# Performance work log

Measured on AMD Instinct MI355X. Metric: run time of the kernel, lower is better.

Reference implementation:

```python
import jax, jax.numpy as jnp
import numpy as np

N, E, D, L, G = 50000, 600000, 128, 3, 512
MAX_DIS = 5
BN_EPS = 1e-5


def _bn(z, g, b):
    # BatchNorm1d in training mode: biased batch statistics over axis 0
    mu = jnp.mean(z, axis=0)
    var = jnp.var(z, axis=0)
    return (z - mu) * jax.lax.rsqrt(var + BN_EPS) * g + b


def setup_inputs() -> dict:
    key = jax.random.key(0)
    ks = jax.random.split(key, 16)
    s = 0.05
    inp = {
        # int inputs
        'd': jax.random.randint(ks[0], (N,), 0, MAX_DIS + 1, dtype=jnp.int32),
        'src': jax.random.randint(ks[1], (E,), 0, N, dtype=jnp.int32),
        'dst': jax.random.randint(ks[2], (E,), 0, N, dtype=jnp.int32),
        'batch_ids': jnp.sort(jax.random.randint(ks[3], (N,), 0, G, dtype=jnp.int32)),
        # NodeEmbedding distance table
        'embed_d': jax.random.normal(ks[4], (MAX_DIS + 1, D)) * s,
        # per-layer params (stacked over L layers)
        'lin_W': jax.random.normal(ks[5], (L, D, D)) * s,   # self.linear weight (stored [in,out])
        'lin_b': jnp.zeros((L, D)),                          # self.linear bias
        'mlp_W1': jax.random.normal(ks[6], (L, D, D)) * s,   # MLP input linear (no bias, norm=True)
        'mlp_g1': jnp.ones((L, D)), 'mlp_b1': jnp.zeros((L, D)),  # MLP inner BN
        'mlp_W2': jax.random.normal(ks[7], (L, D, D)) * s,   # MLP output linear (no bias)
        'eps': jnp.zeros((L,)),                              # GIN eps per layer
        'bn_g': jnp.ones((L, D)), 'bn_b': jnp.zeros((L, D)), # LWL outer BN
        # Pool (gin=False, task='g')
        'pool_W1': jax.random.normal(ks[8], (D, D)) * s,
        'pool_g1': jnp.ones((D,)), 'pool_b1': jnp.zeros((D,)),
        'pool_W2': jax.random.normal(ks[9], (D, D)) * s,
        'pbn_g': jnp.ones((D,)), 'pbn_b': jnp.zeros((D,)),
        # predict MLP (norm=False -> biases, hdim=2*D, odim=num_tasks*num_classes=1)
        'pred_W1': jax.random.normal(ks[10], (D, 2 * D)) * s,
        'pred_b1': jnp.zeros((2 * D,)),
        'pred_W2': jax.random.normal(ks[11], (2 * D, 1)) * s,
        'pred_b2': jnp.zeros((1,)),
    }
    return inp


def reference(d, src, dst, batch_ids, embed_d, lin_W, lin_b,
              mlp_W1, mlp_g1, mlp_b1, mlp_W2, eps, bn_g, bn_b,
              pool_W1, pool_g1, pool_b1, pool_W2, pbn_g, pbn_b,
              pred_W1, pred_b1, pred_W2, pred_b2):
    # NodeEmbedding: x = embed_d(clamp(d, 0, max_dis))  (enc_a=None -> no feature encoder)
    x = embed_d[jnp.clip(d, 0, MAX_DIS)]                      # [N, D]

    counts = jax.ops.segment_sum(jnp.ones((N,), x.dtype), batch_ids, num_segments=G)
    denom = jnp.maximum(counts, 1.0)[:, None]                 # [G, 1]

    h_means = []
    for l in range(L):
        # L('vL'): message = relu(index_select(linear(x), src))  (enc_e=None)
        m = jax.nn.relu((x @ lin_W[l] + lin_b[l])[src])        # [E, D]
        # aggregate = scatter_add to dst over N nodes
        agg = jax.ops.segment_sum(m, dst, num_segments=N)      # [N, D]
        z = x * (1.0 + eps[l]) + agg                           # GIN eps residual
        # MLP(norm=True): Linear(no bias) -> BN -> ReLU -> Linear(no bias)
        h = jax.nn.relu(_bn(z @ mlp_W1[l], mlp_g1[l], mlp_b1[l])) @ mlp_W2[l]
        # LWL outer: x = relu(bn(xL))
        x = jax.nn.relu(_bn(h, bn_g[l], bn_b[l]))
        # global_mean_pool of this layer's output
        h_means.append(jax.ops.segment_sum(x, batch_ids, num_segments=G) / denom)

    # Pool (gin=False, task='g'); index_u is identity for plain MP, so scatter/gather are no-ops
    p = jax.nn.relu(_bn(x @ pool_W1, pool_g1, pool_b1)) @ pool_W2   # pooling MLP
    p = jax.nn.relu(_bn(p, pbn_g, pbn_b))
    h_graph = jax.ops.segment_sum(p, batch_ids, num_segments=G) / denom  # scatter mean
    # predict MLP (norm=False): Linear+bias -> ReLU -> Linear+bias
    prediction = jax.nn.relu(h_graph @ pred_W1 + pred_b1) @ pred_W2 + pred_b2  # [G, 1]

    return prediction, h_graph, jnp.stack(h_means)  # h_list stacked [L, G, D]
```

## Files before the change

### kernel.cpp

```cpp
#include <hip/hip_runtime.h>

typedef unsigned short ushort_t;
typedef __attribute__((ext_vector_type(8))) short bf16x8;
typedef __attribute__((ext_vector_type(4))) float f32x4;

#define NN 50000
#define NE 600000
#define DD 128
#define LL 3
#define GG 512
#define NB_SCAN 98
#define GGRID 1563
#define SBK 32

__device__ __forceinline__ float b2f(ushort_t u){ return __uint_as_float(((unsigned)u)<<16); }
__device__ __forceinline__ ushort_t f2b(float f){
    unsigned x = __float_as_uint(f);
    return (ushort_t)((x + 0x7fffu + ((x>>16)&1u)) >> 16);
}

__global__ void k_mark(float* __restrict__ out, float val, int n){
    int i = blockIdx.x*256 + threadIdx.x; if (i >= n) return;
    out[i] = (i == 0) ? val : 0.f;
}

struct WPtrs { const float* p[11]; };
__global__ void k_setup(WPtrs wp, ushort_t* __restrict__ Wf,
                        const int* __restrict__ bids, int* __restrict__ goff,
                        int* __restrict__ cnt, float* __restrict__ banks,
                        const float* __restrict__ emb, const float* __restrict__ linW,
                        const float* __restrict__ linB, float* __restrict__ yrows){
    int idx = blockIdx.x*256 + threadIdx.x;
    if (idx < 180224){
        int m = idx >> 14, r = idx & 16383;
        int i = r & 7, l2 = (r >> 3) & 63, s = (r >> 9) & 3, n = r >> 11;
        int k   = s*32 + (l2 >> 4)*8 + i;
        int col = n*16 + (l2 & 15);
        Wf[idx] = f2b(wp.p[m][k*DD + col]);
    } else if (idx < 180737){
        int g = idx - 180224;
        int lo = 0, hi = NN;
        while (lo < hi){ int mid = (lo+hi) >> 1; if (bids[mid] < g) lo = mid+1; else hi = mid; }
        goff[g] = lo;
    } else if (idx < 230737){
        cnt[idx - 180737] = 0;
    } else if (idx < 296273){
        banks[idx - 230737] = 0.f;
    } else if (idx < 297041){
        int i = idx - 296273;
        int di = i >> 7, c = i & 127;
        float acc = linB[c];
        for (int k = 0; k < DD; k++) acc = fmaf(emb[di*DD + k], linW[k*DD + c], acc);
        yrows[i] = fmaxf(acc, 0.f);
    }
}

__global__ void k_count(const int* __restrict__ dst, int* __restrict__ cnt){
    int e4 = blockIdx.x*256 + threadIdx.x; if (e4 >= NE/4) return;
    int4 dv = ((const int4*)dst)[e4];
    atomicAdd(&cnt[dv.x], 1); atomicAdd(&cnt[dv.y], 1);
    atomicAdd(&cnt[dv.z], 1); atomicAdd(&cnt[dv.w], 1);
}
__global__ void k_scanA(const int* __restrict__ cnt, int* __restrict__ inc, int* __restrict__ bsum){
    __shared__ int s[512];
    int i = blockIdx.x*512 + threadIdx.x;
    int v = (i < NN) ? cnt[i] : 0;
    s[threadIdx.x] = v; __syncthreads();
    for (int off = 1; off < 512; off <<= 1){
        int add = (threadIdx.x >= off) ? s[threadIdx.x - off] : 0;
        __syncthreads();
        s[threadIdx.x] += add;
        __syncthreads();
    }
    if (i < NN) inc[i] = s[threadIdx.x];
    if (threadIdx.x == 511) bsum[blockIdx.x] = s[511];
}
__global__ void k_scanB(const int* __restrict__ bsum, int* __restrict__ boff){
    __shared__ int s[128];
    int t = threadIdx.x;
    int v = (t < NB_SCAN) ? bsum[t] : 0;
    s[t] = v; __syncthreads();
    for (int off = 1; off < 128; off <<= 1){
        int a = (t >= off) ? s[t - off] : 0;
        __syncthreads();
        s[t] += a;
        __syncthreads();
    }
    if (t < NB_SCAN) boff[t] = s[t] - v;
    if (t == NB_SCAN - 1) boff[NB_SCAN] = s[t];
}
__global__ void k_scanC(const int* __restrict__ cnt, const int* __restrict__ inc,
                        const int* __restrict__ boff, int* __restrict__ rowptr,
                        int* __restrict__ cursor){
    int i = blockIdx.x*512 + threadIdx.x;
    if (i < NN){
        int e = boff[blockIdx.x] + inc[i] - cnt[i];
        rowptr[i] = e; cursor[i] = e;
    } else if (i == NN){
        rowptr[NN] = NE;
    }
}
__global__ void k_fill(const int* __restrict__ src, const int* __restrict__ dst,
                       int* __restrict__ cursor, int* __restrict__ eidx){
    int e4 = blockIdx.x*256 + threadIdx.x; if (e4 >= NE/4) return;
    int4 dv = ((const int4*)dst)[e4];
    int4 sv = ((const int4*)src)[e4];
    int p0 = atomicAdd(&cursor[dv.x], 1); eidx[p0] = sv.x;
    int p1 = atomicAdd(&cursor[dv.y], 1); eidx[p1] = sv.y;
    int p2 = atomicAdd(&cursor[dv.z], 1); eidx[p2] = sv.z;
    int p3 = atomicAdd(&cursor[dv.w], 1); eidx[p3] = sv.w;
}

__global__ void k_agg0(const int* __restrict__ d, const float* __restrict__ emb,
                       const float* __restrict__ yrows,
                       const int* __restrict__ rowptr, const int* __restrict__ eidx,
                       const float* __restrict__ epsP, ushort_t* __restrict__ zb){
    __shared__ float eL[6*DD], yL[6*DD];
    int t = threadIdx.x;
    for (int i = t; i < 6*DD; i += 256){ eL[i] = emb[i]; yL[i] = yrows[i]; }
    __syncthreads();
    int node = blockIdx.x*16 + (t >> 4);
    if (node >= NN) return;
    int c8 = (t & 15) << 3;
    float epl = 1.0f + epsP[0];
    int dv = d[node]; dv = dv < 0 ? 0 : (dv > 5 ? 5 : dv);
    float a[8];
#pragma unroll
    for (int i = 0; i < 8; i++) a[i] = eL[dv*DD + c8 + i] * epl;
    int e0 = rowptr[node], e1 = rowptr[node+1];
    int e = e0;
    for (; e + 3 < e1; e += 4){
        int s0 = eidx[e], s1 = eidx[e+1], s2 = eidx[e+2], s3 = eidx[e+3];
        int c0 = d[s0], c1 = d[s1], c2 = d[s2], c3 = d[s3];
        c0 = c0 < 0 ? 0 : (c0 > 5 ? 5 : c0);
        c1 = c1 < 0 ? 0 : (c1 > 5 ? 5 : c1);
        c2 = c2 < 0 ? 0 : (c2 > 5 ? 5 : c2);
        c3 = c3 < 0 ? 0 : (c3 > 5 ? 5 : c3);
#pragma unroll
        for (int i = 0; i < 8; i++)
            a[i] += (yL[c0*DD + c8 + i] + yL[c1*DD + c8 + i])
                  + (yL[c2*DD + c8 + i] + yL[c3*DD + c8 + i]);
    }
    for (; e < e1; e++){
        int s = eidx[e];
        int c = d[s]; c = c < 0 ? 0 : (c > 5 ? 5 : c);
#pragma unroll
        for (int i = 0; i < 8; i++) a[i] += yL[c*DD + c8 + i];
    }
    bf16x8 o;
#pragma unroll
    for (int i = 0; i < 8; i++) o[i] = (short)f2b(a[i]);
    *(bf16x8*)(zb + (size_t)node*DD + c8) = o;
}

__global__ void k_agg(const ushort_t* __restrict__ xb, const ushort_t* __restrict__ yb,
                      ushort_t* __restrict__ zb,
                      const int* __restrict__ rowptr, const int* __restrict__ eidx,
                      const float* __restrict__ epsP, int l,
                      const float* __restrict__ banksIn, const float* __restrict__ bng,
                      const float* __restrict__ bnb){
    __shared__ float sst[256];
    int t = threadIdx.x;
    {
        float sv = 0.f;
#pragma unroll
        for (int b = 0; b < SBK; b++) sv += banksIn[(b << 8) + t];
        sst[t] = sv;
    }
    __syncthreads();
    int node = blockIdx.x*16 + (t >> 4);
    if (node >= NN) return;
    int c8 = (t & 15) << 3;
    float epl = 1.0f + epsP[l];
    bf16x8 xr = *(const bf16x8*)(xb + (size_t)node*DD + c8);
    float a[8];
#pragma unroll
    for (int i = 0; i < 8; i++){
        int c = c8 + i;
        float mu  = sst[c] * (1.0f/NN);
        float var = sst[c + DD] * (1.0f/NN) - mu*mu;
        float sc  = rsqrtf(fmaxf(var, 0.f) + 1e-5f) * bng[c];
        float sh  = bnb[c] - mu*sc;
        a[i] = fmaxf(fmaf(b2f((ushort_t)xr[i]), sc, sh), 0.f) * epl;
    }
    int e0 = rowptr[node], e1 = rowptr[node+1];
    int e = e0;
    for (; e + 3 < e1; e += 4){
        int s0 = eidx[e], s1 = eidx[e+1], s2 = eidx[e+2], s3 = eidx[e+3];
        bf16x8 v0 = *(const bf16x8*)(yb + (size_t)s0*DD + c8);
        bf16x8 v1 = *(const bf16x8*)(yb + (size_t)s1*DD + c8);
        bf16x8 v2 = *(const bf16x8*)(yb + (size_t)s2*DD + c8);
        bf16x8 v3 = *(const bf16x8*)(yb + (size_t)s3*DD + c8);
#pragma unroll
        for (int i = 0; i < 8; i++)
            a[i] += (b2f((ushort_t)v0[i]) + b2f((ushort_t)v1[i]))
                  + (b2f((ushort_t)v2[i]) + b2f((ushort_t)v3[i]));
    }
    for (; e < e1; e++){
        int s = eidx[e];
        bf16x8 v = *(const bf16x8*)(yb + (size_t)s*DD + c8);
#pragma unroll
        for (int i = 0; i < 8; i++) a[i] += b2f((ushort_t)v[i]);
    }
    bf16x8 o;
#pragma unroll
    for (int i = 0; i < 8; i++) o[i] = (short)f2b(a[i]);
    *(bf16x8*)(zb + (size_t)node*DD + c8) = o;
}

template<int AMODE, int OMODE, int STATS, int POOL>
__global__ __launch_bounds__(256) void k_gemm(
    const ushort_t* __restrict__ A, const ushort_t* __restrict__ Wf,
    const float* __restrict__ bias,
    const float* __restrict__ banksIn, const float* __restrict__ bng,
    const float* __restrict__ bnb,
    ushort_t* __restrict__ C, float* __restrict__ banksOut,
    const int* __restrict__ goff, float* __restrict__ pool_out, int M)
{
    __shared__ float ssl[256];
    __shared__ float sred[256];
    __shared__ ushort_t lrep[32*132];
    const int t = threadIdx.x;

    if (POOL && blockIdx.x >= GGRID){
        int g = blockIdx.x - GGRID;
        {
            float sv = 0.f;
#pragma unroll
            for (int b = 0; b < SBK; b++) sv += banksIn[(b << 8) + t];
            ssl[t] = sv;
        }
        __syncthreads();
        int c = t & 127, hf = t >> 7;
        float mu  = ssl[c] * (1.0f/NN);
        float var = ssl[c + DD] * (1.0f/NN) - mu*mu;
        float sc  = rsqrtf(fmaxf(var, 0.f) + 1e-5f) * bng[c];
        float sh  = bnb[c] - mu*sc;
        int r0 = goff[g], r1 = goff[g+1];
        float acc = 0.f;
        for (int r = r0 + hf; r < r1; r += 2)
            acc += fmaxf(fmaf(b2f(A[(size_t)r*DD + c]), sc, sh), 0.f);
        sred[t] = acc; __syncthreads();
        if (t < 128)
            pool_out[g*DD + t] = (sred[t] + sred[t+128]) / fmaxf((float)(r1 - r0), 1.0f);
        return;
    }

    const int w = t >> 6, l = t & 63;
    const int rw = w >> 1, cw = w & 1;
    const int rowBlk = blockIdx.x*32, rowBase = rowBlk + rw*16;
    const int lm = l & 15, kg = l >> 4;

    if (AMODE == 2){
        float sv = 0.f;
#pragma unroll
        for (int b = 0; b < SBK; b++) sv += banksIn[(b << 8) + t];
        ssl[t] = sv;
        __syncthreads();
        if (t < 128){
            float mu  = ssl[t] * (1.0f/NN);
            float var = ssl[t + DD] * (1.0f/NN) - mu*mu;
            float sc  = rsqrtf(fmaxf(var, 0.f) + 1e-5f) * bng[t];
            ssl[t] = sc;
            ssl[t + DD] = bnb[t] - mu*sc;
        }
    }
    if (STATS) sred[t] = 0.f;
    if (AMODE == 2 || STATS) __syncthreads();

    f32x4 acc[4];
#pragma unroll
    for (int n = 0; n < 4; n++) acc[n] = (f32x4){0.f,0.f,0.f,0.f};

    int arow = rowBase + lm;
    if (arow >= M) arow = M - 1;
    const ushort_t* aptr = A + (size_t)arow*DD + kg*8;

#pragma unroll
    for (int s = 0; s < 4; s++){
        bf16x8 af;
        if (AMODE == 0){
            af = *(const bf16x8*)(aptr + s*32);
        } else {
            bf16x8 ar = *(const bf16x8*)(aptr + s*32);
            int k0 = s*32 + kg*8;
#pragma unroll
            for (int i = 0; i < 8; i++){
                float v = b2f((ushort_t)ar[i]);
                v = fmaxf(fmaf(v, ssl[k0+i], ssl[DD+k0+i]), 0.f);
                ((ushort_t*)&af)[i] = f2b(v);
            }
        }
#pragma unroll
        for (int n = 0; n < 4; n++){
            int nc = cw*4 + n;
            bf16x8 bfr = *(const bf16x8*)(Wf + (size_t)((nc*4 + s)*64 + l)*8);
            acc[n] = __builtin_amdgcn_mfma_f32_16x16x32_bf16(af, bfr, acc[n], 0, 0, 0);
        }
    }

#pragma unroll
    for (int n = 0; n < 4; n++){
        int col = (cw*4 + n)*16 + lm;
        float cs = 0.f, cq = 0.f;
#pragma unroll
        for (int j = 0; j < 4; j++){
            float v = acc[n][j];
            if (OMODE == 1) v = fmaxf(v + bias[col], 0.f);
            lrep[(rw*16 + kg*4 + j)*132 + col] = f2b(v);
            if (STATS && (rowBase + kg*4 + j) < M){ cs += v; cq += v*v; }
        }
        if (STATS){
            cs += __shfl_xor(cs, 16); cs += __shfl_xor(cs, 32);
            cq += __shfl_xor(cq, 16); cq += __shfl_xor(cq, 32);
            if (kg == 0){
                atomicAdd(&sred[col], cs);
                atomicAdd(&sred[col + DD], cq);
            }
        }
    }
    __syncthreads();

    {
        int lr = t >> 3;
        int gr = rowBlk + lr;
        if (gr < M){
            int seg = (t & 7) * 16;
            const ushort_t* lp = lrep + lr*132 + seg;
            bf16x8 o0 = *(const bf16x8*)(lp);
            bf16x8 o1 = *(const bf16x8*)(lp + 8);
            ushort_t* cp = C + (size_t)gr*DD + seg;
            *(bf16x8*)(cp)     = o0;
            *(bf16x8*)(cp + 8) = o1;
        }
    }

    if (STATS){
        __syncthreads();
        atomicAdd(&banksOut[((blockIdx.x & (SBK-1)) << 8) + t], sred[t]);
    }
}

__global__ __launch_bounds__(256) void k_poolpred(const ushort_t* __restrict__ zb,
        const float* __restrict__ banksIn, const float* __restrict__ bng,
        const float* __restrict__ bnb, const int* __restrict__ goff,
        const float* __restrict__ W1, const float* __restrict__ b1,
        const float* __restrict__ W2, const float* __restrict__ b2,
        float* __restrict__ out_hgraph, float* __restrict__ out_pred){
    __shared__ float hrow[DD];
    __shared__ float pr[256];
    int g = blockIdx.x, t = threadIdx.x;
    {
        float sv = 0.f;
#pragma unroll
        for (int b = 0; b < SBK; b++) sv += banksIn[(b << 8) + t];
        pr[t] = sv;
    }
    __syncthreads();
    int c = t & 127, hf = t >> 7;
    float mu  = pr[c] * (1.0f/NN);
    float var = pr[c + DD] * (1.0f/NN) - mu*mu;
    float sc  = rsqrtf(fmaxf(var, 0.f) + 1e-5f) * bng[c];
    float sh  = bnb[c] - mu*sc;
    __syncthreads();
    int r0 = goff[g], r1 = goff[g+1];
    float acc = 0.f;
    for (int r = r0 + hf; r < r1; r += 2)
        acc += fmaxf(fmaf(b2f(zb[(size_t)r*DD + c]), sc, sh), 0.f);
    pr[t] = acc; __syncthreads();
    if (t < 128){
        float m = (pr[t] + pr[t+128]) / fmaxf((float)(r1 - r0), 1.0f);
        hrow[t] = m;
        out_hgraph[g*DD + t] = m;
    }
    __syncthreads();
    float a2 = b1[t];
    for (int k = 0; k < DD; k++) a2 = fmaf(hrow[k], W1[k*256 + t], a2);
    pr[t] = fmaxf(a2, 0.f) * W2[t];
    __syncthreads();
    for (int off = 128; off > 0; off >>= 1){
        if (t < off) pr[t] += pr[t + off];
        __syncthreads();
    }
    if (t == 0) out_pred[g] = pr[0] + b2[0];
}

extern "C" void kernel_launch(void* const* d_in, const int* in_sizes, int n_in,
                              void* d_out, int out_size, void* d_ws, size_t ws_size,
                              hipStream_t stream){
    float* out = (float*)d_out;
    const int OUT_N = GG + GG*DD + LL*GG*DD;

    static const int EXP[24] = {50000,600000,600000,50000, 768,49152,384,49152,384,384,
                                49152,3,384,384,16384,128,128,16384,128,128,
                                32768,256,256,1};
    int bad = -1;
    if (n_in != 24) bad = 50;
    else for (int i = 0; i < 24; i++) if (in_sizes[i] != EXP[i]) { bad = i; break; }
    if (bad >= 0){
        k_mark<<<(OUT_N+255)/256, 256, 0, stream>>>(out, 2048.0f + (float)bad, OUT_N);
        return;
    }

    const int* d    = (const int*)d_in[0];
    const int* src  = (const int*)d_in[1];
    const int* dst  = (const int*)d_in[2];
    const int* bids = (const int*)d_in[3];
    const float* emb  = (const float*)d_in[4];
    const float* linW = (const float*)d_in[5];
    const float* linB = (const float*)d_in[6];
    const float* W1   = (const float*)d_in[7];
    const float* g1   = (const float*)d_in[8];
    const float* b1   = (const float*)d_in[9];
    const float* W2   = (const float*)d_in[10];
    const float* epsA = (const float*)d_in[11];
    const float* bng  = (const float*)d_in[12];
    const float* bnb  = (const float*)d_in[13];
    const float* pW1  = (const float*)d_in[14];
    const float* pg1  = (const float*)d_in[15];
    const float* pb1  = (const float*)d_in[16];
    const float* pW2  = (const float*)d_in[17];
    const float* pbng = (const float*)d_in[18];
    const float* pbnb = (const float*)d_in[19];
    const float* prW1 = (const float*)d_in[20];
    const float* prb1 = (const float*)d_in[21];
    const float* prW2 = (const float*)d_in[22];
    const float* prb2 = (const float*)d_in[23];

    ushort_t* xb  = (ushort_t*)d_ws;
    ushort_t* yb  = xb + (size_t)NN*DD;
    ushort_t* zb  = yb + (size_t)NN*DD;
    ushort_t* Wf  = zb + (size_t)NN*DD;
    float* SBANKS= (float*)(Wf + 11*16384);
    float* yrows = SBANKS + 8*SBK*256;
    int* cnt    = (int*)(yrows + 6*DD);
    int* inc    = cnt + NN;
    int* rowptr = inc + NN;
    int* cursor = rowptr + NN + 1;
    int* eidx   = cursor + NN;
    int* goff   = eidx + NE;
    int* bsum   = goff + GG + 1;
    int* boff   = bsum + NB_SCAN;

    float* out_pred   = out;
    float* out_hgraph = out + GG;
    float* out_hmeans = out + GG + GG*DD;

    const int AGG_GRID  = (NN + 15)/16;
    const int E4_GRID   = (NE/4 + 255)/256;
    const int SETUP_GRID= (297041 + 255)/256;
    const int GP_GRID   = GGRID + GG;

    WPtrs wp;
    for (int i = 0; i < 3; i++){
        wp.p[i]   = linW + (size_t)i*DD*DD;
        wp.p[3+i] = W1   + (size_t)i*DD*DD;
        wp.p[6+i] = W2   + (size_t)i*DD*DD;
    }
    wp.p[9] = pW1; wp.p[10] = pW2;
    const ushort_t* WfLin = Wf;
    const ushort_t* WfW1  = Wf + 3*16384;
    const ushort_t* WfW2  = Wf + 6*16384;
    const ushort_t* WfPW1 = Wf + 9*16384;
    const ushort_t* WfPW2 = Wf + 10*16384;

    float* BK0 = SBANKS + 0*SBK*256;
    float* BK1 = SBANKS + 1*SBK*256;
    float* BK5 = SBANKS + 5*SBK*256;
    float* BK6 = SBANKS + 6*SBK*256;
    float* BK7 = SBANKS + 7*SBK*256;

    k_setup<<<SETUP_GRID, 256, 0, stream>>>(wp, Wf, bids, goff, cnt, SBANKS,
                                            emb, linW, linB, yrows);
    k_count<<<E4_GRID, 256, 0, stream>>>(dst, cnt);
    k_scanA<<<NB_SCAN, 512, 0, stream>>>(cnt, inc, bsum);
    k_scanB<<<1, 128, 0, stream>>>(bsum, boff);
    k_scanC<<<NB_SCAN, 512, 0, stream>>>(cnt, inc, boff, rowptr, cursor);
    k_fill<<<E4_GRID, 256, 0, stream>>>(src, dst, cursor, eidx);

    k_agg0<<<AGG_GRID, 256, 0, stream>>>(d, emb, yrows, rowptr, eidx, epsA, zb);
    k_gemm<0,0,1,0><<<GGRID, 256, 0, stream>>>(zb, WfW1, nullptr, nullptr, nullptr, nullptr,
        yb, BK0, nullptr, nullptr, NN);
    k_gemm<2,0,1,0><<<GGRID, 256, 0, stream>>>(yb, WfW2, nullptr, BK0, g1, b1,
        xb, BK1, nullptr, nullptr, NN);

    for (int l = 1; l < LL; l++){
        float* pbank = SBANKS + (size_t)(2*l - 1)*SBK*256;
        float* bIn   = SBANKS + (size_t)(2*l)*SBK*256;
        float* bOut  = SBANKS + (size_t)(2*l + 1)*SBK*256;
        const float* pg = bng + (size_t)(l-1)*DD;
        const float* pb = bnb + (size_t)(l-1)*DD;

        k_gemm<2,1,0,1><<<GP_GRID, 256, 0, stream>>>(xb, WfLin + (size_t)l*16384,
            linB + (size_t)l*DD, pbank, pg, pb,
            yb, nullptr, goff, out_hmeans + (size_t)(l-1)*GG*DD, NN);
        k_agg<<<AGG_GRID, 256, 0, stream>>>(xb, yb, zb, rowptr, eidx, epsA, l, pbank, pg, pb);
        k_gemm<0,0,1,0><<<GGRID, 256, 0, stream>>>(zb, WfW1 + (size_t)l*16384, nullptr,
            nullptr, nullptr, nullptr, yb, bIn, nullptr, nullptr, NN);
        k_gemm<2,0,1,0><<<GGRID, 256, 0, stream>>>(yb, WfW2 + (size_t)l*16384, nullptr,
            bIn, g1 + (size_t)l*DD, b1 + (size_t)l*DD, xb, bOut, nullptr, nullptr, NN);
    }

    k_gemm<2,0,1,1><<<GP_GRID, 256, 0, stream>>>(xb, WfPW1, nullptr,
        BK5, bng + 2*DD, bnb + 2*DD,
        yb, BK6, goff, out_hmeans + (size_t)2*GG*DD, NN);
    k_gemm<2,0,1,0><<<GGRID, 256, 0, stream>>>(yb, WfPW2, nullptr,
        BK6, pg1, pb1, zb, BK7, nullptr, nullptr, NN);
    k_poolpred<<<GG, 256, 0, stream>>>(zb, BK7, pbng, pbnb, goff,
        prW1, prb1, prW2, prb2, out_hgraph, out_pred);
}
```

Baseline: 372.3 us.

## Fuse neighbor aggregation into first MLP GEMM and merge scan kernels

The separate aggregation kernels (layer 0 lookup-table path and later bf16 gather path) are folded into the W1 GEMM. Each block gathers and sums neighbor messages for its 32 rows into LDS, then feeds them to the MFMA. This removes the z round trip through global memory and two launches per layer. The scanB kernel is merged into scanC by having every block redo the small 98-element prefix scan. In exchange the GEMM blocks carry more LDS and irregular gather latency, which may lower occupancy, and buffers are re-routed (zb/yb swapped).

New measurement: 358.0 us. 3.8% less time.

```diff
diff --git a/kernel.cpp b/kernel.cpp
--- a/kernel.cpp
+++ b/kernel.cpp
@@ -75,26 +75,23 @@
     if (i < NN) inc[i] = s[threadIdx.x];
     if (threadIdx.x == 511) bsum[blockIdx.x] = s[511];
 }
-__global__ void k_scanB(const int* __restrict__ bsum, int* __restrict__ boff){
-    __shared__ int s[128];
+__global__ void k_scanC(const int* __restrict__ cnt, const int* __restrict__ inc,
+                        const int* __restrict__ bsum, int* __restrict__ rowptr,
+                        int* __restrict__ cursor){
+    __shared__ int sb[128];
     int t = threadIdx.x;
-    int v = (t < NB_SCAN) ? bsum[t] : 0;
-    s[t] = v; __syncthreads();
+    if (t < 128) sb[t] = (t < NB_SCAN) ? bsum[t] : 0;
+    __syncthreads();
     for (int off = 1; off < 128; off <<= 1){
-        int a = (t >= off) ? s[t - off] : 0;
-        __syncthreads();
-        s[t] += a;
-        __syncthreads();
-    }
-    if (t < NB_SCAN) boff[t] = s[t] - v;
-    if (t == NB_SCAN - 1) boff[NB_SCAN] = s[t];
-}
-__global__ void k_scanC(const int* __restrict__ cnt, const int* __restrict__ inc,
-                        const int* __restrict__ boff, int* __restrict__ rowptr,
-                        int* __restrict__ cursor){
-    int i = blockIdx.x*512 + threadIdx.x;
+        int a = (t < 128 && t >= off) ? sb[t - off] : 0;
+        __syncthreads();
+        if (t < 128) sb[t] += a;
+        __syncthreads();
+    }
+    int myoff = (blockIdx.x == 0) ? 0 : sb[blockIdx.x - 1];
+    int i = blockIdx.x*512 + t;
     if (i < NN){
-        int e = boff[blockIdx.x] + inc[i] - cnt[i];
+        int e = myoff + inc[i] - cnt[i];
         rowptr[i] = e; cursor[i] = e;
     } else if (i == NN){
         rowptr[NN] = NE;
@@ -111,115 +108,24 @@
     int p3 = atomicAdd(&cursor[dv.w], 1); eidx[p3] = sv.w;
 }
 
-__global__ void k_agg0(const int* __restrict__ d, const float* __restrict__ emb,
-                       const float* __restrict__ yrows,
-                       const int* __restrict__ rowptr, const int* __restrict__ eidx,
-                       const float* __restrict__ epsP, ushort_t* __restrict__ zb){
-    __shared__ float eL[6*DD], yL[6*DD];
-    int t = threadIdx.x;
-    for (int i = t; i < 6*DD; i += 256){ eL[i] = emb[i]; yL[i] = yrows[i]; }
-    __syncthreads();
-    int node = blockIdx.x*16 + (t >> 4);
-    if (node >= NN) return;
-    int c8 = (t & 15) << 3;
-    float epl = 1.0f + epsP[0];
-    int dv = d[node]; dv = dv < 0 ? 0 : (dv > 5 ? 5 : dv);
-    float a[8];
-#pragma unroll
-    for (int i = 0; i < 8; i++) a[i] = eL[dv*DD + c8 + i] * epl;
-    int e0 = rowptr[node], e1 = rowptr[node+1];
-    int e = e0;
-    for (; e + 3 < e1; e += 4){
-        int s0 = eidx[e], s1 = eidx[e+1], s2 = eidx[e+2], s3 = eidx[e+3];
-        int c0 = d[s0], c1 = d[s1], c2 = d[s2], c3 = d[s3];
-        c0 = c0 < 0 ? 0 : (c0 > 5 ? 5 : c0);
-        c1 = c1 < 0 ? 0 : (c1 > 5 ? 5 : c1);
-        c2 = c2 < 0 ? 0 : (c2 > 5 ? 5 : c2);
-        c3 = c3 < 0 ? 0 : (c3 > 5 ? 5 : c3);
-#pragma unroll
-        for (int i = 0; i < 8; i++)
-            a[i] += (yL[c0*DD + c8 + i] + yL[c1*DD + c8 + i])
-                  + (yL[c2*DD + c8 + i] + yL[c3*DD + c8 + i]);
-    }
-    for (; e < e1; e++){
-        int s = eidx[e];
-        int c = d[s]; c = c < 0 ? 0 : (c > 5 ? 5 : c);
-#pragma unroll
-        for (int i = 0; i < 8; i++) a[i] += yL[c*DD + c8 + i];
-    }
-    bf16x8 o;
-#pragma unroll
-    for (int i = 0; i < 8; i++) o[i] = (short)f2b(a[i]);
-    *(bf16x8*)(zb + (size_t)node*DD + c8) = o;
-}
-
-__global__ void k_agg(const ushort_t* __restrict__ xb, const ushort_t* __restrict__ yb,
-                      ushort_t* __restrict__ zb,
-                      const int* __restrict__ rowptr, const int* __restrict__ eidx,
-                      const float* __restrict__ epsP, int l,
-                      const float* __restrict__ banksIn, const float* __restrict__ bng,
-                      const float* __restrict__ bnb){
-    __shared__ float sst[256];
-    int t = threadIdx.x;
-    {
-        float sv = 0.f;
-#pragma unroll
-        for (int b = 0; b < SBK; b++) sv += banksIn[(b << 8) + t];
-        sst[t] = sv;
-    }
-    __syncthreads();
-    int node = blockIdx.x*16 + (t >> 4);
-    if (node >= NN) return;
-    int c8 = (t & 15) << 3;
-    float epl = 1.0f + epsP[l];
-    bf16x8 xr = *(const bf16x8*)(xb + (size_t)node*DD + c8);
-    float a[8];
-#pragma unroll
-    for (int i = 0; i < 8; i++){
-        int c = c8 + i;
-        float mu  = sst[c] * (1.0f/NN);
-        float var = sst[c + DD] * (1.0f/NN) - mu*mu;
-        float sc  = rsqrtf(fmaxf(var, 0.f) + 1e-5f) * bng[c];
-        float sh  = bnb[c] - mu*sc;
-        a[i] = fmaxf(fmaf(b2f((ushort_t)xr[i]), sc, sh), 0.f) * epl;
-    }
-    int e0 = rowptr[node], e1 = rowptr[node+1];
-    int e = e0;
-    for (; e + 3 < e1; e += 4){
-        int s0 = eidx[e], s1 = eidx[e+1], s2 = eidx[e+2], s3 = eidx[e+3];
-        bf16x8 v0 = *(const bf16x8*)(yb + (size_t)s0*DD + c8);
-        bf16x8 v1 = *(const bf16x8*)(yb + (size_t)s1*DD + c8);
-        bf16x8 v2 = *(const bf16x8*)(yb + (size_t)s2*DD + c8);
-        bf16x8 v3 = *(const bf16x8*)(yb + (size_t)s3*DD + c8);
-#pragma unroll
-        for (int i = 0; i < 8; i++)
-            a[i] += (b2f((ushort_t)v0[i]) + b2f((ushort_t)v1[i]))
-                  + (b2f((ushort_t)v2[i]) + b2f((ushort_t)v3[i]));
-    }
-    for (; e < e1; e++){
-        int s = eidx[e];
-        bf16x8 v = *(const bf16x8*)(yb + (size_t)s*DD + c8);
-#pragma unroll
-        for (int i = 0; i < 8; i++) a[i] += b2f((ushort_t)v[i]);
-    }
-    bf16x8 o;
-#pragma unroll
-    for (int i = 0; i < 8; i++) o[i] = (short)f2b(a[i]);
-    *(bf16x8*)(zb + (size_t)node*DD + c8) = o;
-}
-
-template<int AMODE, int OMODE, int STATS, int POOL>
+template<int AM, int OM, int ST, int POOL>
 __global__ __launch_bounds__(256) void k_gemm(
     const ushort_t* __restrict__ A, const ushort_t* __restrict__ Wf,
     const float* __restrict__ bias,
     const float* __restrict__ banksIn, const float* __restrict__ bng,
     const float* __restrict__ bnb,
+    const ushort_t* __restrict__ msg,
+    const int* __restrict__ rowptr, const int* __restrict__ eidx,
+    const int* __restrict__ darr, const float* __restrict__ emb6,
+    const float* __restrict__ yrows, const float* __restrict__ epsP, int lidx,
     ushort_t* __restrict__ C, float* __restrict__ banksOut,
     const int* __restrict__ goff, float* __restrict__ pool_out, int M)
 {
     __shared__ float ssl[256];
     __shared__ float sred[256];
     __shared__ ushort_t lrep[32*132];
+    __shared__ ushort_t zlds[(AM >= 3) ? 32*132 : 1];
+    __shared__ float luts[(AM == 4) ? 2*6*132 : 1];
     const int t = threadIdx.x;
 
     if (POOL && blockIdx.x >= GGRID){
@@ -251,7 +157,7 @@
     const int rowBlk = blockIdx.x*32, rowBase = rowBlk + rw*16;
     const int lm = l & 15, kg = l >> 4;
 
-    if (AMODE == 2){
+    if (AM == 2 || AM == 3){
         float sv = 0.f;
 #pragma unroll
         for (int b = 0; b < SBK; b++) sv += banksIn[(b << 8) + t];
@@ -265,8 +171,75 @@
             ssl[t + DD] = bnb[t] - mu*sc;
         }
     }
-    if (STATS) sred[t] = 0.f;
-    if (AMODE == 2 || STATS) __syncthreads();
+    if (AM == 4){
+        for (int i = t; i < 6*DD; i += 256){
+            int r6 = i >> 7, c = i & 127;
+            luts[r6*132 + c]         = yrows[i];
+            luts[6*132 + r6*132 + c] = emb6[i];
+        }
+    }
+    if (ST) sred[t] = 0.f;
+    __syncthreads();
+
+    if (AM == 3 || AM == 4){
+        int row  = t >> 3;
+        int cseg = (t & 7) * 16;
+        int grow = rowBlk + row; if (grow >= M) grow = M - 1;
+        float epl = 1.0f + epsP[lidx];
+        float z[16];
+        if (AM == 3){
+            const ushort_t* xp = A + (size_t)grow*DD + cseg;
+            bf16x8 x0 = *(const bf16x8*)(xp);
+            bf16x8 x1 = *(const bf16x8*)(xp + 8);
+#pragma unroll
+            for (int i = 0; i < 8; i++){
+                z[i]   = fmaxf(fmaf(b2f((ushort_t)x0[i]), ssl[cseg+i],   ssl[DD+cseg+i]),   0.f) * epl;
+                z[8+i] = fmaxf(fmaf(b2f((ushort_t)x1[i]), ssl[cseg+8+i], ssl[DD+cseg+8+i]), 0.f) * epl;
+            }
+        } else {
+            int dv = darr[grow]; dv = dv < 0 ? 0 : (dv > 5 ? 5 : dv);
+            const float* ep = luts + 6*132 + dv*132 + cseg;
+#pragma unroll
+            for (int i = 0; i < 16; i++) z[i] = ep[i] * epl;
+        }
+        int e0 = rowptr[grow], e1 = rowptr[grow+1];
+        if (AM == 3){
+            int e = e0;
+            for (; e + 1 < e1; e += 2){
+                int s0 = eidx[e], s1 = eidx[e+1];
+                const ushort_t* m0 = msg + (size_t)s0*DD + cseg;
+                const ushort_t* m1 = msg + (size_t)s1*DD + cseg;
+                bf16x8 a0 = *(const bf16x8*)(m0), a1 = *(const bf16x8*)(m0 + 8);
+                bf16x8 b0 = *(const bf16x8*)(m1), b1 = *(const bf16x8*)(m1 + 8);
+#pragma unroll
+                for (int i = 0; i < 8; i++){
+                    z[i]   += b2f((ushort_t)a0[i]) + b2f((ushort_t)b0[i]);
+                    z[8+i] += b2f((ushort_t)a1[i]) + b2f((ushort_t)b1[i]);
+                }
+            }
+            for (; e < e1; e++){
+                int s0 = eidx[e];
+                const ushort_t* m0 = msg + (size_t)s0*DD + cseg;
+                bf16x8 a0 = *(const bf16x8*)(m0), a1 = *(const bf16x8*)(m0 + 8);
+#pragma unroll
+                for (int i = 0; i < 8; i++){
+                    z[i]   += b2f((ushort_t)a0[i]);
+                    z[8+i] += b2f((ushort_t)a1[i]);
+                }
+            }
+        } else {
+            for (int e = e0; e < e1; e++){
+                int di = darr[eidx[e]]; di = di < 0 ? 0 : (di > 5 ? 5 : di);
+                const float* yp = luts + di*132 + cseg;
+#pragma unroll
+                for (int i = 0; i < 16; i++) z[i] += yp[i];
+            }
+        }
+        ushort_t* zp = zlds + row*132 + cseg;
+#pragma unroll
+        for (int i = 0; i < 16; i++) zp[i] = f2b(z[i]);
+        __syncthreads();
+    }
 
     f32x4 acc[4];
 #pragma unroll
@@ -274,28 +247,38 @@
 
     int arow = rowBase + lm;
     if (arow >= M) arow = M - 1;
-    const ushort_t* aptr = A + (size_t)arow*DD + kg*8;
+
+    bf16x8 af[4];
+    if (AM == 3 || AM == 4){
+        const ushort_t* zp = zlds + (rw*16 + lm)*132 + kg*8;
+#pragma unroll
+        for (int s = 0; s < 4; s++) af[s] = *(const bf16x8*)(zp + s*32);
+    } else {
+        const ushort_t* aptr = A + (size_t)arow*DD + kg*8;
+#pragma unroll
+        for (int s = 0; s < 4; s++){
+            bf16x8 ar = *(const bf16x8*)(aptr + s*32);
+            if (AM == 0){
+                af[s] = ar;
+            } else {
+                int k0 = s*32 + kg*8;
+#pragma unroll
+                for (int i = 0; i < 8; i++){
+                    float v = b2f((ushort_t)ar[i]);
+                    v = fmaxf(fmaf(v, ssl[k0+i], ssl[DD+k0+i]), 0.f);
+                    ((ushort_t*)&af[s])[i] = f2b(v);
+                }
+            }
+        }
+    }
 
 #pragma unroll
     for (int s = 0; s < 4; s++){
-        bf16x8 af;
-        if (AMODE == 0){
-            af = *(const bf16x8*)(aptr + s*32);
-        } else {
-            bf16x8 ar = *(const bf16x8*)(aptr + s*32);
-            int k0 = s*32 + kg*8;
-#pragma unroll
-            for (int i = 0; i < 8; i++){
-                float v = b2f((ushort_t)ar[i]);
-                v = fmaxf(fmaf(v, ssl[k0+i], ssl[DD+k0+i]), 0.f);
-                ((ushort_t*)&af)[i] = f2b(v);
-            }
-        }
 #pragma unroll
         for (int n = 0; n < 4; n++){
             int nc = cw*4 + n;
             bf16x8 bfr = *(const bf16x8*)(Wf + (size_t)((nc*4 + s)*64 + l)*8);
-            acc[n] = __builtin_amdgcn_mfma_f32_16x16x32_bf16(af, bfr, acc[n], 0, 0, 0);
+            acc[n] = __builtin_amdgcn_mfma_f32_16x16x32_bf16(af[s], bfr, acc[n], 0, 0, 0);
         }
     }
 
@@ -306,11 +289,11 @@
 #pragma unroll
         for (int j = 0; j < 4; j++){
             float v = acc[n][j];
-            if (OMODE == 1) v = fmaxf(v + bias[col], 0.f);
+            if (OM == 1) v = fmaxf(v + bias[col], 0.f);
             lrep[(rw*16 + kg*4 + j)*132 + col] = f2b(v);
-            if (STATS && (rowBase + kg*4 + j) < M){ cs += v; cq += v*v; }
-        }
-        if (STATS){
+            if (ST && (rowBase + kg*4 + j) < M){ cs += v; cq += v*v; }
+        }
+        if (ST){
             cs += __shfl_xor(cs, 16); cs += __shfl_xor(cs, 32);
             cq += __shfl_xor(cq, 16); cq += __shfl_xor(cq, 32);
             if (kg == 0){
@@ -335,7 +318,7 @@
         }
     }
 
-    if (STATS){
+    if (ST){
         __syncthreads();
         atomicAdd(&banksOut[((blockIdx.x & (SBK-1)) << 8) + t], sred[t]);
     }
@@ -440,13 +423,11 @@
     int* eidx   = cursor + NN;
     int* goff   = eidx + NE;
     int* bsum   = goff + GG + 1;
-    int* boff   = bsum + NB_SCAN;
 
     float* out_pred   = out;
     float* out_hgraph = out + GG;
     float* out_hmeans = out + GG + GG*DD;
 
-    const int AGG_GRID  = (NN + 15)/16;
     const int E4_GRID   = (NE/4 + 255)/256;
     const int SETUP_GRID= (297041 + 255)/256;
     const int GP_GRID   = GGRID + GG;
@@ -474,14 +455,15 @@
                                             emb, linW, linB, yrows);
     k_count<<<E4_GRID, 256, 0, stream>>>(dst, cnt);
     k_scanA<<<NB_SCAN, 512, 0, stream>>>(cnt, inc, bsum);
-    k_scanB<<<1, 128, 0, stream>>>(bsum, boff);
-    k_scanC<<<NB_SCAN, 512, 0, stream>>>(cnt, inc, boff, rowptr, cursor);
+    k_scanC<<<NB_SCAN, 512, 0, stream>>>(cnt, inc, bsum, rowptr, cursor);
     k_fill<<<E4_GRID, 256, 0, stream>>>(src, dst, cursor, eidx);
 
-    k_agg0<<<AGG_GRID, 256, 0, stream>>>(d, emb, yrows, rowptr, eidx, epsA, zb);
-    k_gemm<0,0,1,0><<<GGRID, 256, 0, stream>>>(zb, WfW1, nullptr, nullptr, nullptr, nullptr,
+    k_gemm<4,0,1,0><<<GGRID, 256, 0, stream>>>(nullptr, WfW1, nullptr,
+        nullptr, nullptr, nullptr,
+        nullptr, rowptr, eidx, d, emb, yrows, epsA, 0,
         yb, BK0, nullptr, nullptr, NN);
     k_gemm<2,0,1,0><<<GGRID, 256, 0, stream>>>(yb, WfW2, nullptr, BK0, g1, b1,
+        nullptr, nullptr, nullptr, nullptr, nullptr, nullptr, nullptr, 0,
         xb, BK1, nullptr, nullptr, NN);
 
     for (int l = 1; l < LL; l++){
@@ -493,19 +475,26 @@
 
         k_gemm<2,1,0,1><<<GP_GRID, 256, 0, stream>>>(xb, WfLin + (size_t)l*16384,
             linB + (size_t)l*DD, pbank, pg, pb,
+            nullptr, nullptr, nullptr, nullptr, nullptr, nullptr, nullptr, 0,
             yb, nullptr, goff, out_hmeans + (size_t)(l-1)*GG*DD, NN);
-        k_agg<<<AGG_GRID, 256, 0, stream>>>(xb, yb, zb, rowptr, eidx, epsA, l, pbank, pg, pb);
-        k_gemm<0,0,1,0><<<GGRID, 256, 0, stream>>>(zb, WfW1 + (size_t)l*16384, nullptr,
-            nullptr, nullptr, nullptr, yb, bIn, nullptr, nullptr, NN);
-        k_gemm<2,0,1,0><<<GGRID, 256, 0, stream>>>(yb, WfW2 + (size_t)l*16384, nullptr,
-            bIn, g1 + (size_t)l*DD, b1 + (size_t)l*DD, xb, bOut, nullptr, nullptr, NN);
+        k_gemm<3,0,1,0><<<GGRID, 256, 0, stream>>>(xb, WfW1 + (size_t)l*16384, nullptr,
+            pbank, pg, pb,
+            yb, rowptr, eidx, nullptr, nullptr, nullptr, epsA, l,
+            zb, bIn, nullptr, nullptr, NN);
+        k_gemm<2,0,1,0><<<GGRID, 256, 0, stream>>>(zb, WfW2 + (size_t)l*16384, nullptr,
+            bIn, g1 + (size_t)l*DD, b1 + (size_t)l*DD,
+            nullptr, nullptr, nullptr, nullptr, nullptr, nullptr, nullptr, 0,
+            xb, bOut, nullptr, nullptr, NN);
     }
 
     k_gemm<2,0,1,1><<<GP_GRID, 256, 0, stream>>>(xb, WfPW1, nullptr,
         BK5, bng + 2*DD, bnb + 2*DD,
+        nullptr, nullptr, nullptr, nullptr, nullptr, nullptr, nullptr, 0,
         yb, BK6, goff, out_hmeans + (size_t)2*GG*DD, NN);
     k_gemm<2,0,1,0><<<GGRID, 256, 0, stream>>>(yb, WfPW2, nullptr,
-        BK6, pg1, pb1, zb, BK7, nullptr, nullptr, NN);
+        BK6, pg1, pb1,
+        nullptr, nullptr, nullptr, nullptr, nullptr, nullptr, nullptr, 0,
+        zb, BK7, nullptr, nullptr, NN);
     k_poolpred<<<GG, 256, 0, stream>>>(zb, BK7, pbng, pbnb, goff,
         prW1, prb1, prW2, prb2, out_hgraph, out_pred);
 }
```
